# Performance work log

Measured on AMD Instinct MI355X. Metric: run time of the kernel, lower is better.

Reference implementation:

```python
import jax, jax.numpy as jnp
import numpy as np

EPS = 1e-5
TAU = 2.0
HEADS = 8
SCALE = 0.125


def _bn(y, g, b, m, v):
    # y: [TB, C, N]; per-channel eval-mode batchnorm
    inv = jax.lax.rsqrt(v + EPS)
    return (y - m[:, None]) * (g * inv)[:, None] + b[:, None]


def _lif(x_seq, vth):
    # spikingjelly MultiStepLIFNode: v += (x - v)/tau, spike = H(v - vth), hard reset v*(1-s)
    def step(mem, xt):
        mem = mem + (xt - mem) / TAU
        s = (mem >= vth).astype(xt.dtype)
        mem = mem * (1.0 - s)
        return mem, s
    _, spikes = jax.lax.scan(step, jnp.zeros_like(x_seq[0]), x_seq)
    return spikes


def setup_inputs() -> dict:
    key = jax.random.key(0)
    ks = jax.random.split(key, 8)
    T, B, C, H, W = 4, 16, 256, 32, 32
    d = {
        'x': jax.random.normal(ks[0], (T, B, C, H, W), jnp.float32),
        'res_attn': jnp.zeros((1,), jnp.float32),
    }
    for i, p in enumerate(['q', 'k', 'v']):
        d[p + '_w'] = jax.random.normal(ks[1 + i], (C, C), jnp.float32) * 0.02
        d[p + '_gamma'] = jnp.ones((C,), jnp.float32)
        d[p + '_beta'] = jnp.zeros((C,), jnp.float32)
        d[p + '_mean'] = jnp.zeros((C,), jnp.float32)
        d[p + '_var'] = jnp.ones((C,), jnp.float32)
    d['p_w'] = jax.random.normal(ks[4], (C, C), jnp.float32) * 0.02
    d['p_b'] = jnp.zeros((C,), jnp.float32)
    d['p_gamma'] = jnp.ones((C,), jnp.float32)
    d['p_beta'] = jnp.zeros((C,), jnp.float32)
    d['p_mean'] = jnp.zeros((C,), jnp.float32)
    d['p_var'] = jnp.ones((C,), jnp.float32)
    return d


def reference(x, res_attn, q_w, q_gamma, q_beta, q_mean, q_var,
              k_w, k_gamma, k_beta, k_mean, k_var,
              v_w, v_gamma, v_beta, v_mean, v_var,
              p_w, p_b, p_gamma, p_beta, p_mean, p_var):
    T, B, C, H, W = x.shape
    N = H * W
    d = C // HEADS
    x2 = x.reshape(T * B, C, N)

    def branch(w, g, b, m, v):
        y = _bn(jnp.einsum('oc,bcn->bon', w, x2), g, b, m, v).reshape(T, B, C, N)
        s = _lif(y, 1.0)  # [T,B,C,N]
        # -> [T,B,heads,N,d]
        return s.transpose(0, 1, 3, 2).reshape(T, B, N, HEADS, d).transpose(0, 1, 3, 2, 4)

    q = branch(q_w, q_gamma, q_beta, q_mean, q_var)
    k = branch(k_w, k_gamma, k_beta, k_mean, k_var)
    v = branch(v_w, v_gamma, v_beta, v_mean, v_var)

    kv = jnp.einsum('tbhnd,tbhne->tbhde', k, v)      # [T,B,h,d,d]
    attn = jnp.einsum('tbhnd,tbhde->tbhne', q, kv) * SCALE  # [T,B,h,N,d]
    xa = attn.transpose(0, 1, 2, 4, 3).reshape(T, B, C, N)
    xa = _lif(xa, 0.5)

    y = _bn(jnp.einsum('oc,bcn->bon', p_w, xa.reshape(T * B, C, N)) + p_b[:, None],
            p_gamma, p_beta, p_mean, p_var)
    out = _lif(y.reshape(T, B, C, H, W), 1.0)
    return (out, v)
```

## Files before the change

### kernel.cpp

```cpp
#include <hip/hip_runtime.h>
#include <stdint.h>

typedef unsigned int u32;
typedef unsigned short ushort_t;

#define T_ 4
#define B_ 16
#define C_ 256
#define N_ 1024
#define CN (C_ * N_)
#define M_ELEMS (64 * C_ * N_)

#define OFF_S    0ull
#define OFF_YP   0ull
#define OFF_XC   67108864ull
#define OFF_SC   67108864ull
#define OFF_KV   134217728ull
#define OFF_BNS  136314880ull
#define OFF_WC   136331264ull
#define OFF_WPC  137510912ull

typedef __attribute__((ext_vector_type(8))) short bf16x8;
typedef __attribute__((ext_vector_type(4))) float f32x4;

__device__ __forceinline__ ushort_t f2bf(float f) {
  u32 u = __float_as_uint(f);
  u32 r = (u + 0x7FFFu + ((u >> 16) & 1u)) >> 16;
  return (ushort_t)r;
}
__device__ __forceinline__ float bf2f(ushort_t h) { return __uint_as_float((u32)h << 16); }

__device__ __forceinline__ void async_copy16(const void* g, void* l) {
  __builtin_amdgcn_global_load_lds(
      (const __attribute__((address_space(1))) u32*)g,
      (__attribute__((address_space(3))) u32*)l, 16, 0, 0);
}

__device__ __forceinline__ void mfma_grp(const ushort_t* Ap, int aoff,
                                         bf16x8 b0, bf16x8 b1, bf16x8 b2, bf16x8 b3,
                                         f32x4* acc) {
  bf16x8 a0 = *(const bf16x8*)&Ap[aoff + 0 * 16 * 32];
  bf16x8 a1 = *(const bf16x8*)&Ap[aoff + 1 * 16 * 32];
  bf16x8 a2 = *(const bf16x8*)&Ap[aoff + 2 * 16 * 32];
  bf16x8 a3 = *(const bf16x8*)&Ap[aoff + 3 * 16 * 32];
  acc[0]  = __builtin_amdgcn_mfma_f32_16x16x32_bf16(a0, b0, acc[0],  0, 0, 0);
  acc[1]  = __builtin_amdgcn_mfma_f32_16x16x32_bf16(a0, b1, acc[1],  0, 0, 0);
  acc[2]  = __builtin_amdgcn_mfma_f32_16x16x32_bf16(a0, b2, acc[2],  0, 0, 0);
  acc[3]  = __builtin_amdgcn_mfma_f32_16x16x32_bf16(a0, b3, acc[3],  0, 0, 0);
  acc[4]  = __builtin_amdgcn_mfma_f32_16x16x32_bf16(a1, b0, acc[4],  0, 0, 0);
  acc[5]  = __builtin_amdgcn_mfma_f32_16x16x32_bf16(a1, b1, acc[5],  0, 0, 0);
  acc[6]  = __builtin_amdgcn_mfma_f32_16x16x32_bf16(a1, b2, acc[6],  0, 0, 0);
  acc[7]  = __builtin_amdgcn_mfma_f32_16x16x32_bf16(a1, b3, acc[7],  0, 0, 0);
  acc[8]  = __builtin_amdgcn_mfma_f32_16x16x32_bf16(a2, b0, acc[8],  0, 0, 0);
  acc[9]  = __builtin_amdgcn_mfma_f32_16x16x32_bf16(a2, b1, acc[9],  0, 0, 0);
  acc[10] = __builtin_amdgcn_mfma_f32_16x16x32_bf16(a2, b2, acc[10], 0, 0, 0);
  acc[11] = __builtin_amdgcn_mfma_f32_16x16x32_bf16(a2, b3, acc[11], 0, 0, 0);
  acc[12] = __builtin_amdgcn_mfma_f32_16x16x32_bf16(a3, b0, acc[12], 0, 0, 0);
  acc[13] = __builtin_amdgcn_mfma_f32_16x16x32_bf16(a3, b1, acc[13], 0, 0, 0);
  acc[14] = __builtin_amdgcn_mfma_f32_16x16x32_bf16(a3, b2, acc[14], 0, 0, 0);
  acc[15] = __builtin_amdgcn_mfma_f32_16x16x32_bf16(a3, b3, acc[15], 0, 0, 0);
}

__global__ void bn_prep(const float* __restrict__ qg, const float* __restrict__ qb2, const float* __restrict__ qm, const float* __restrict__ qv,
                        const float* __restrict__ kg, const float* __restrict__ kb, const float* __restrict__ km, const float* __restrict__ kvv,
                        const float* __restrict__ vg, const float* __restrict__ vb, const float* __restrict__ vm, const float* __restrict__ vv,
                        const float* __restrict__ pbias,
                        const float* __restrict__ pg, const float* __restrict__ pbt, const float* __restrict__ pm, const float* __restrict__ pv,
                        float* __restrict__ bns) {
  int i = threadIdx.x;
  int br = i >> 8, c = i & 255;
  const float *g, *bt, *m, *v;
  float bias = 0.f;
  if (br == 0)      { g = qg; bt = qb2; m = qm; v = qv; }
  else if (br == 1) { g = kg; bt = kb;  m = km; v = kvv; }
  else if (br == 2) { g = vg; bt = vb;  m = vm; v = vv; }
  else              { g = pg; bt = pbt; m = pm; v = pv; bias = pbias[c]; }
  float sc = g[c] / sqrtf(v[c] + 1e-5f);
  float sh = bt[c] + (bias - m[c]) * sc;
  float rcp = (sc != 0.f) ? (1.f / sc) : 0.f;
  *(float4*)&bns[4 * i] = make_float4(sc, sh, rcp, 0.f);
}

__global__ __launch_bounds__(256) void convert_w(const float* __restrict__ qw, const float* __restrict__ kw,
                                                 const float* __restrict__ vw, const float* __restrict__ pw,
                                                 ushort_t* __restrict__ Wc, ushort_t* __restrict__ Wpc) {
  int id = blockIdx.x * 256 + threadIdx.x;
  int br = id >> 16, o = (id >> 8) & 255, c = id & 255;
  const float* w = (br == 0) ? qw : (br == 1) ? kw : (br == 2) ? vw : pw;
  float f = w[o * 256 + c];
  ushort_t hi = f2bf(f);
  ushort_t lo = f2bf(f - bf2f(hi));
  if (br < 3) {
    ushort_t* d = Wc + (size_t)br * 196608 + (size_t)o * 768 + c;
    d[0] = hi; d[256] = lo; d[512] = hi;
  } else {
    ushort_t* d = Wpc + (size_t)o * 512 + c;
    d[0] = hi; d[256] = lo;
  }
}

__global__ __launch_bounds__(256) void convert_x(const float* __restrict__ x, ushort_t* __restrict__ Xc) {
  __shared__ ushort_t hi[32][260];
  __shared__ ushort_t lo[32][260];
  int bid = blockIdx.x;
  int nc = bid & 3, kb = (bid >> 2) & 7, tb = bid >> 5;
  int t = threadIdx.x;
  int n0 = nc * 256;
  const float* xb = x + (size_t)tb * CN + (size_t)(kb * 32) * N_ + n0;
#pragma unroll
  for (int p = 0; p < 8; ++p) {
    int k = p * 4 + (t >> 6);
    int n4 = (t & 63) * 4;
    float4 v = *(const float4*)&xb[(size_t)k * N_ + n4];
    ushort_t h0 = f2bf(v.x), h1 = f2bf(v.y), h2 = f2bf(v.z), h3 = f2bf(v.w);
    short4 hv = make_short4((short)h0, (short)h1, (short)h2, (short)h3);
    short4 lv = make_short4((short)f2bf(v.x - bf2f(h0)), (short)f2bf(v.y - bf2f(h1)),
                            (short)f2bf(v.z - bf2f(h2)), (short)f2bf(v.w - bf2f(h3)));
    *(short4*)&hi[k][n4] = hv;
    *(short4*)&lo[k][n4] = lv;
  }
  __syncthreads();
  ushort_t* Hs = Xc + ((size_t)(tb * 16 + kb) * 1024 + n0) * 32;
  ushort_t* Ls = Xc + ((size_t)(tb * 16 + 8 + kb) * 1024 + n0) * 32;
  int kq = t & 3;
#pragma unroll
  for (int q = 0; q < 4; ++q) {
    int n = q * 64 + (t >> 2);
    u32 a0 = (u32)hi[kq * 8 + 0][n] | ((u32)hi[kq * 8 + 1][n] << 16);
    u32 a1 = (u32)hi[kq * 8 + 2][n] | ((u32)hi[kq * 8 + 3][n] << 16);
    u32 a2 = (u32)hi[kq * 8 + 4][n] | ((u32)hi[kq * 8 + 5][n] << 16);
    u32 a3 = (u32)hi[kq * 8 + 6][n] | ((u32)hi[kq * 8 + 7][n] << 16);
    *(uint4*)(Hs + (size_t)n * 32 + kq * 8) = make_uint4(a0, a1, a2, a3);
    u32 b0 = (u32)lo[kq * 8 + 0][n] | ((u32)lo[kq * 8 + 1][n] << 16);
    u32 b1 = (u32)lo[kq * 8 + 2][n] | ((u32)lo[kq * 8 + 3][n] << 16);
    u32 b2 = (u32)lo[kq * 8 + 4][n] | ((u32)lo[kq * 8 + 5][n] << 16);
    u32 b3 = (u32)lo[kq * 8 + 6][n] | ((u32)lo[kq * 8 + 7][n] << 16);
    *(uint4*)(Ls + (size_t)n * 32 + kq * 8) = make_uint4(b0, b1, b2, b3);
  }
}

__global__ __launch_bounds__(256, 3) void gemm_qkv_lif(
    const ushort_t* __restrict__ Wc, const ushort_t* __restrict__ Xc,
    const float* __restrict__ bns, uint8_t* __restrict__ S) {
  __shared__ ushort_t Ah[2][4096];
  __shared__ ushort_t Xl[2][4096];
  __shared__ ushort_t Bh[2][4096];
  const int nt = blockIdx.x, mt = blockIdx.y, b = blockIdx.z;
  const int br = mt >> 1, rh = mt & 1;
  const ushort_t* Ab = Wc + (size_t)br * 196608 + (size_t)(rh * 128) * 768;
  const int tid = threadIdx.x;
  const int lane = tid & 63;
  const int quad = lane >> 4, r = lane & 15;
  const int w = tid >> 6;
  const int moff = (w & 1) * 64, noff = (w >> 1) * 64;
  const int c0 = tid, c1 = tid + 256;
  const int aoff = (moff + r) * 32 + quad * 8;
  const int boff = (noff + r) * 32 + quad * 8;

  f32x4 acc[16];
#pragma unroll
  for (int f = 0; f < 16; ++f) acc[f] = (f32x4){0.f, 0.f, 0.f, 0.f};

  for (int t = 0; t < 4; ++t) {
    const ushort_t* Xtb = Xc + (size_t)(t * 16 + b) * 16 * 32768 + (size_t)(nt * 128) * 32;
    for (int p = 0; p < 4; ++p) {
      const ushort_t* AcH = Ab + p * 64;
      const ushort_t* AcL = Ab + 256 + p * 64;
      const ushort_t* Bh0 = Xtb + (size_t)(2 * p) * 32768;
      const ushort_t* Bh1 = Bh0 + 32768;
      async_copy16(AcH + (size_t)(c0 >> 2) * 768 + (c0 & 3) * 8,      &Ah[0][c0 * 8]);
      async_copy16(AcH + (size_t)(c1 >> 2) * 768 + (c1 & 3) * 8,      &Ah[0][c1 * 8]);
      async_copy16(AcH + (size_t)(c0 >> 2) * 768 + 32 + (c0 & 3) * 8, &Ah[1][c0 * 8]);
      async_copy16(AcH + (size_t)(c1 >> 2) * 768 + 32 + (c1 & 3) * 8, &Ah[1][c1 * 8]);
      async_copy16(AcL + (size_t)(c0 >> 2) * 768 + (c0 & 3) * 8,      &Xl[0][c0 * 8]);
      async_copy16(AcL + (size_t)(c1 >> 2) * 768 + (c1 & 3) * 8,      &Xl[0][c1 * 8]);
      async_copy16(AcL + (size_t)(c0 >> 2) * 768 + 32 + (c0 & 3) * 8, &Xl[1][c0 * 8]);
      async_copy16(AcL + (size_t)(c1 >> 2) * 768 + 32 + (c1 & 3) * 8, &Xl[1][c1 * 8]);
      async_copy16(Bh0 + c0 * 8, &Bh[0][c0 * 8]);
      async_copy16(Bh0 + c1 * 8, &Bh[0][c1 * 8]);
      async_copy16(Bh1 + c0 * 8, &Bh[1][c0 * 8]);
      async_copy16(Bh1 + c1 * 8, &Bh[1][c1 * 8]);
      __syncthreads();
      {
        bf16x8 b0 = *(const bf16x8*)&Bh[0][boff + 0 * 16 * 32];
        bf16x8 b1 = *(const bf16x8*)&Bh[0][boff + 1 * 16 * 32];
        bf16x8 b2 = *(const bf16x8*)&Bh[0][boff + 2 * 16 * 32];
        bf16x8 b3 = *(const bf16x8*)&Bh[0][boff + 3 * 16 * 32];
        mfma_grp(&Ah[0][0], aoff, b0, b1, b2, b3, acc);
        mfma_grp(&Xl[0][0], aoff, b0, b1, b2, b3, acc);
      }
      {
        bf16x8 b0 = *(const bf16x8*)&Bh[1][boff + 0 * 16 * 32];
        bf16x8 b1 = *(const bf16x8*)&Bh[1][boff + 1 * 16 * 32];
        bf16x8 b2 = *(const bf16x8*)&Bh[1][boff + 2 * 16 * 32];
        bf16x8 b3 = *(const bf16x8*)&Bh[1][boff + 3 * 16 * 32];
        mfma_grp(&Ah[1][0], aoff, b0, b1, b2, b3, acc);
        mfma_grp(&Xl[1][0], aoff, b0, b1, b2, b3, acc);
      }
      __syncthreads();
      const ushort_t* Bl0 = Xtb + (size_t)(8 + 2 * p) * 32768;
      const ushort_t* Bl1 = Bl0 + 32768;
      async_copy16(Bl0 + c0 * 8, &Xl[0][c0 * 8]);
      async_copy16(Bl0 + c1 * 8, &Xl[0][c1 * 8]);
      async_copy16(Bl1 + c0 * 8, &Xl[1][c0 * 8]);
      async_copy16(Bl1 + c1 * 8, &Xl[1][c1 * 8]);
      __syncthreads();
      {
        bf16x8 b0 = *(const bf16x8*)&Xl[0][boff + 0 * 16 * 32];
        bf16x8 b1 = *(const bf16x8*)&Xl[0][boff + 1 * 16 * 32];
        bf16x8 b2 = *(const bf16x8*)&Xl[0][boff + 2 * 16 * 32];
        bf16x8 b3 = *(const bf16x8*)&Xl[0][boff + 3 * 16 * 32];
        mfma_grp(&Ah[0][0], aoff, b0, b1, b2, b3, acc);
      }
      {
        bf16x8 b0 = *(const bf16x8*)&Xl[1][boff + 0 * 16 * 32];
        bf16x8 b1 = *(const bf16x8*)&Xl[1][boff + 1 * 16 * 32];
        bf16x8 b2 = *(const bf16x8*)&Xl[1][boff + 2 * 16 * 32];
        bf16x8 b3 = *(const bf16x8*)&Xl[1][boff + 3 * 16 * 32];
        mfma_grp(&Ah[1][0], aoff, b0, b1, b2, b3, acc);
      }
      __syncthreads();
    }
    uint8_t* Sb = S + (size_t)br * M_ELEMS + (size_t)(t * 16 + b) * CN;
#pragma unroll
    for (int i = 0; i < 4; ++i) {
#pragma unroll
      for (int rg = 0; rg < 4; ++rg) {
        int c = rh * 128 + moff + i * 16 + quad * 4 + rg;
        float4 bn = *(const float4*)&bns[4 * (br * 256 + c)];
        float hsc = 0.5f * bn.x;
        float hsh = 0.5f * bn.y;
        float rcp = bn.z;
        uint8_t* row = Sb + (size_t)c * N_ + nt * 128 + noff + r;
#pragma unroll
        for (int j = 0; j < 4; ++j) {
          float m = acc[i * 4 + j][rg] * hsc + hsh;
          uint8_t s = (m >= 1.0f) ? 1 : 0;
          row[j * 16] = s;
          acc[i * 4 + j][rg] = s ? 0.f : m * rcp;
        }
      }
    }
  }
}

__global__ __launch_bounds__(256) void transpose_v(const uint8_t* __restrict__ SV, float* __restrict__ vout) {
  size_t o4 = ((size_t)blockIdx.x * 256 + threadIdx.x) * 4;
  int dd = (int)(o4 & 31);
  int n = (int)((o4 >> 5) & 1023);
  int h = (int)((o4 >> 15) & 7);
  int tb = (int)(o4 >> 18);
  const uint8_t* src = SV + (size_t)tb * CN + (size_t)(h * 32 + dd) * N_ + n;
  *(float4*)(vout + o4) = make_float4((float)src[0], (float)src[(size_t)N_],
                                      (float)src[2 * (size_t)N_], (float)src[3 * (size_t)N_]);
}

__global__ __launch_bounds__(256) void kv_gram(const uint8_t* __restrict__ SK,
                                               const uint8_t* __restrict__ SV,
                                               float* __restrict__ KV) {
  __shared__ uint8_t Ks[32 * 132];
  __shared__ uint8_t Vs[32 * 132];
  const int tb = blockIdx.x >> 3, h = blockIdx.x & 7;
  const uint8_t* K = SK + (size_t)tb * CN + (size_t)h * 32 * N_;
  const uint8_t* V = SV + (size_t)tb * CN + (size_t)h * 32 * N_;
  const int tid = threadIdx.x;
  const int dd = tid >> 3, e0 = (tid & 7) * 4;
  const int lr = tid >> 3, lc = (tid & 7) * 16;
  float a0 = 0.f, a1 = 0.f, a2 = 0.f, a3 = 0.f;
  for (int n0 = 0; n0 < N_; n0 += 128) {
    uint4 kk4 = *(const uint4*)(K + (size_t)lr * N_ + n0 + lc);
    uint4 vv4 = *(const uint4*)(V + (size_t)lr * N_ + n0 + lc);
    unsigned* Kw = (unsigned*)(Ks + lr * 132 + lc);
    unsigned* Vw = (unsigned*)(Vs + lr * 132 + lc);
    Kw[0] = kk4.x; Kw[1] = kk4.y; Kw[2] = kk4.z; Kw[3] = kk4.w;
    Vw[0] = vv4.x; Vw[1] = vv4.y; Vw[2] = vv4.z; Vw[3] = vv4.w;
    __syncthreads();
    for (int n = 0; n < 128; ++n) {
      float kf = (float)Ks[dd * 132 + n];
      a0 += kf * (float)Vs[(e0 + 0) * 132 + n];
      a1 += kf * (float)Vs[(e0 + 1) * 132 + n];
      a2 += kf * (float)Vs[(e0 + 2) * 132 + n];
      a3 += kf * (float)Vs[(e0 + 3) * 132 + n];
    }
    __syncthreads();
  }
  float* o = KV + (size_t)(tb * 8 + h) * 1024 + dd * 32 + e0;
  o[0] = a0; o[1] = a1; o[2] = a2; o[3] = a3;
}

__global__ __launch_bounds__(256) void attn_lif(const uint8_t* __restrict__ SQ,
                                                const float* __restrict__ KV,
                                                ushort_t* __restrict__ Sc) {
  __shared__ float kvs[1024];
  const int bid = blockIdx.x;
  const int nb = bid & 15, h = (bid >> 4) & 7, b = bid >> 7;
  const int n0 = nb * 64;
  const int tid = threadIdx.x;
  const int nl = tid & 63, eg = tid >> 6;
  float mem[8];
#pragma unroll
  for (int j = 0; j < 8; ++j) mem[j] = 0.f;
  for (int t = 0; t < 4; ++t) {
    const float* kvp = KV + (size_t)((t * B_ + b) * 8 + h) * 1024;
    *(float4*)&kvs[tid * 4] = *(const float4*)&kvp[tid * 4];
    __syncthreads();
    const uint8_t* q = SQ + (size_t)(t * B_ + b) * CN + (size_t)h * 32 * N_ + n0 + nl;
    float val[8];
#pragma unroll
    for (int j = 0; j < 8; ++j) val[j] = 0.f;
#pragma unroll 4
    for (int dd = 0; dd < 32; ++dd) {
      float qv = (float)q[(size_t)dd * N_];
#pragma unroll
      for (int j = 0; j < 8; ++j) val[j] += qv * kvs[dd * 32 + eg * 8 + j];
    }
    ushort_t pk[8];
#pragma unroll
    for (int j = 0; j < 8; ++j) {
      float a = val[j] * 0.125f;
      mem[j] += (a - mem[j]) * 0.5f;
      int s = (mem[j] >= 0.5f);
      pk[j] = s ? (ushort_t)0x3F80 : (ushort_t)0;
      if (s) mem[j] = 0.f;
    }
    uint4 o;
    o.x = (u32)pk[0] | ((u32)pk[1] << 16);
    o.y = (u32)pk[2] | ((u32)pk[3] << 16);
    o.z = (u32)pk[4] | ((u32)pk[5] << 16);
    o.w = (u32)pk[6] | ((u32)pk[7] << 16);
    *(uint4*)(Sc + ((size_t)((t * B_ + b) * 8 + h) * 1024 + n0 + nl) * 32 + eg * 8) = o;
    __syncthreads();
  }
}

__global__ __launch_bounds__(256, 3) void gemm_p_mfma(
    const ushort_t* __restrict__ Wpc, const ushort_t* __restrict__ Sc,
    const float* __restrict__ bns, float* __restrict__ YP) {
  __shared__ ushort_t Ah[2][4096];
  __shared__ ushort_t Al[2][4096];
  __shared__ ushort_t Bs[2][4096];
  const int nt = blockIdx.x, mt = blockIdx.y, tb = blockIdx.z;
  const ushort_t* Ab = Wpc + (size_t)(mt * 128) * 512;
  const int tid = threadIdx.x;
  const int lane = tid & 63;
  const int quad = lane >> 4, r = lane & 15;
  const int w = tid >> 6;
  const int moff = (w & 1) * 64, noff = (w >> 1) * 64;
  const int c0 = tid, c1 = tid + 256;
  const int aoff = (moff + r) * 32 + quad * 8;
  const int boff = (noff + r) * 32 + quad * 8;
  f32x4 acc[16];
#pragma unroll
  for (int f = 0; f < 16; ++f) acc[f] = (f32x4){0.f, 0.f, 0.f, 0.f};
  const ushort_t* Stb = Sc + (size_t)tb * 8 * 32768 + (size_t)(nt * 128) * 32;
  for (int p = 0; p < 4; ++p) {
    const ushort_t* AcH = Ab + p * 64;
    const ushort_t* AcL = Ab + 256 + p * 64;
    const ushort_t* Bb0 = Stb + (size_t)(2 * p) * 32768;
    const ushort_t* Bb1 = Bb0 + 32768;
    async_copy16(AcH + (size_t)(c0 >> 2) * 512 + (c0 & 3) * 8,      &Ah[0][c0 * 8]);
    async_copy16(AcH + (size_t)(c1 >> 2) * 512 + (c1 & 3) * 8,      &Ah[0][c1 * 8]);
    async_copy16(AcH + (size_t)(c0 >> 2) * 512 + 32 + (c0 & 3) * 8, &Ah[1][c0 * 8]);
    async_copy16(AcH + (size_t)(c1 >> 2) * 512 + 32 + (c1 & 3) * 8, &Ah[1][c1 * 8]);
    async_copy16(AcL + (size_t)(c0 >> 2) * 512 + (c0 & 3) * 8,      &Al[0][c0 * 8]);
    async_copy16(AcL + (size_t)(c1 >> 2) * 512 + (c1 & 3) * 8,      &Al[0][c1 * 8]);
    async_copy16(AcL + (size_t)(c0 >> 2) * 512 + 32 + (c0 & 3) * 8, &Al[1][c0 * 8]);
    async_copy16(AcL + (size_t)(c1 >> 2) * 512 + 32 + (c1 & 3) * 8, &Al[1][c1 * 8]);
    async_copy16(Bb0 + c0 * 8, &Bs[0][c0 * 8]);
    async_copy16(Bb0 + c1 * 8, &Bs[0][c1 * 8]);
    async_copy16(Bb1 + c0 * 8, &Bs[1][c0 * 8]);
    async_copy16(Bb1 + c1 * 8, &Bs[1][c1 * 8]);
    __syncthreads();
    {
      bf16x8 b0 = *(const bf16x8*)&Bs[0][boff + 0 * 16 * 32];
      bf16x8 b1 = *(const bf16x8*)&Bs[0][boff + 1 * 16 * 32];
      bf16x8 b2 = *(const bf16x8*)&Bs[0][boff + 2 * 16 * 32];
      bf16x8 b3 = *(const bf16x8*)&Bs[0][boff + 3 * 16 * 32];
      mfma_grp(&Ah[0][0], aoff, b0, b1, b2, b3, acc);
      mfma_grp(&Al[0][0], aoff, b0, b1, b2, b3, acc);
    }
    {
      bf16x8 b0 = *(const bf16x8*)&Bs[1][boff + 0 * 16 * 32];
      bf16x8 b1 = *(const bf16x8*)&Bs[1][boff + 1 * 16 * 32];
      bf16x8 b2 = *(const bf16x8*)&Bs[1][boff + 2 * 16 * 32];
      bf16x8 b3 = *(const bf16x8*)&Bs[1][boff + 3 * 16 * 32];
      mfma_grp(&Ah[1][0], aoff, b0, b1, b2, b3, acc);
      mfma_grp(&Al[1][0], aoff, b0, b1, b2, b3, acc);
    }
    __syncthreads();
  }
  float* Yb = YP + (size_t)tb * CN;
#pragma unroll
  for (int i = 0; i < 4; ++i) {
#pragma unroll
    for (int rg = 0; rg < 4; ++rg) {
      int c = mt * 128 + moff + i * 16 + quad * 4 + rg;
      float4 bn = *(const float4*)&bns[4 * (768 + c)];
      float sc = bn.x;
      float sh = bn.y;
      float* row = Yb + (size_t)c * N_ + nt * 128 + noff + r;
#pragma unroll
      for (int j = 0; j < 4; ++j) row[j * 16] = acc[i * 4 + j][rg] * sc + sh;
    }
  }
}

__global__ __launch_bounds__(256) void lif_out(const float* __restrict__ YP, float* __restrict__ out) {
  size_t e4 = ((size_t)blockIdx.x * 256 + threadIdx.x) * 4;
  float m0 = 0.f, m1 = 0.f, m2 = 0.f, m3 = 0.f;
#pragma unroll
  for (int t = 0; t < 4; ++t) {
    float4 y = *(const float4*)(YP + (size_t)t * (B_ * CN) + e4);
    m0 += (y.x - m0) * 0.5f;
    m1 += (y.y - m1) * 0.5f;
    m2 += (y.z - m2) * 0.5f;
    m3 += (y.w - m3) * 0.5f;
    float s0 = (m0 >= 1.0f) ? 1.f : 0.f;
    float s1 = (m1 >= 1.0f) ? 1.f : 0.f;
    float s2 = (m2 >= 1.0f) ? 1.f : 0.f;
    float s3 = (m3 >= 1.0f) ? 1.f : 0.f;
    *(float4*)(out + (size_t)t * (B_ * CN) + e4) = make_float4(s0, s1, s2, s3);
    m0 *= (1.f - s0);
    m1 *= (1.f - s1);
    m2 *= (1.f - s2);
    m3 *= (1.f - s3);
  }
}

extern "C" void kernel_launch(void* const* d_in, const int* in_sizes, int n_in,
                              void* d_out, int out_size, void* d_ws, size_t ws_size,
                              hipStream_t stream) {
  const float* x   = (const float*)d_in[0];
  const float* qw  = (const float*)d_in[2];
  const float* qg  = (const float*)d_in[3];
  const float* qb  = (const float*)d_in[4];
  const float* qm  = (const float*)d_in[5];
  const float* qv  = (const float*)d_in[6];
  const float* kw  = (const float*)d_in[7];
  const float* kg  = (const float*)d_in[8];
  const float* kb  = (const float*)d_in[9];
  const float* km  = (const float*)d_in[10];
  const float* kvv = (const float*)d_in[11];
  const float* vw  = (const float*)d_in[12];
  const float* vg  = (const float*)d_in[13];
  const float* vb  = (const float*)d_in[14];
  const float* vm  = (const float*)d_in[15];
  const float* vv  = (const float*)d_in[16];
  const float* pw  = (const float*)d_in[17];
  const float* pb  = (const float*)d_in[18];
  const float* pg  = (const float*)d_in[19];
  const float* pbt = (const float*)d_in[20];
  const float* pm  = (const float*)d_in[21];
  const float* pv  = (const float*)d_in[22];

  float* out = (float*)d_out;
  float* vout = out + M_ELEMS;

  uint8_t* ws = (uint8_t*)d_ws;
  uint8_t* S   = ws + OFF_S;
  float* YP    = (float*)(ws + OFF_YP);
  ushort_t* Xc = (ushort_t*)(ws + OFF_XC);
  ushort_t* Sc = (ushort_t*)(ws + OFF_SC);
  float* KV    = (float*)(ws + OFF_KV);
  float* BNS   = (float*)(ws + OFF_BNS);
  ushort_t* Wc  = (ushort_t*)(ws + OFF_WC);
  ushort_t* Wpc = (ushort_t*)(ws + OFF_WPC);

  bn_prep<<<dim3(1), dim3(1024), 0, stream>>>(qg, qb, qm, qv, kg, kb, km, kvv,
                                              vg, vb, vm, vv, pb, pg, pbt, pm, pv, BNS);
  convert_w<<<dim3(1024), dim3(256), 0, stream>>>(qw, kw, vw, pw, Wc, Wpc);
  convert_x<<<dim3(2048), dim3(256), 0, stream>>>(x, Xc);
  gemm_qkv_lif<<<dim3(8, 6, 16), dim3(256), 0, stream>>>(Wc, Xc, BNS, S);
  transpose_v<<<dim3(16384), dim3(256), 0, stream>>>(S + 2ull * M_ELEMS, vout);
  kv_gram<<<dim3(512), dim3(256), 0, stream>>>(S + 1ull * M_ELEMS, S + 2ull * M_ELEMS, KV);
  attn_lif<<<dim3(2048), dim3(256), 0, stream>>>(S, KV, Sc);
  gemm_p_mfma<<<dim3(8, 2, 64), dim3(256), 0, stream>>>(Wpc, Sc, BNS, YP);
  lif_out<<<dim3(4096), dim3(256), 0, stream>>>(YP, out);
}
```

Measured before the change: 433.9 us.

## Fuse output LIF into projection GEMM and bit-pack spikes for KV gram

The projection GEMM now loops over the four timesteps inside one block per batch and applies BN plus the LIF recurrence in its epilogue, keeping membrane state in the accumulators. This removes the fp32 YP intermediate round trip and the separate lif_out kernel. The kv_gram kernel packs byte spikes into 64-bit bitmasks and computes K^T V with AND plus popcount instead of a float loop over bytes. The trade-off is a GEMM grid four times smaller (256 blocks), which may underfill the GPU. The fused epilogue also relies on the bns table holding a reciprocal scale in its z field to carry the membrane between timesteps.

```diff
diff --git a/kernel.cpp b/kernel.cpp
--- a/kernel.cpp
+++ b/kernel.cpp
@@ -12,7 +12,6 @@
 #define M_ELEMS (64 * C_ * N_)
 
 #define OFF_S    0ull
-#define OFF_YP   0ull
 #define OFF_XC   67108864ull
 #define OFF_SC   67108864ull
 #define OFF_KV   134217728ull
@@ -258,34 +257,36 @@
 __global__ __launch_bounds__(256) void kv_gram(const uint8_t* __restrict__ SK,
                                                const uint8_t* __restrict__ SV,
                                                float* __restrict__ KV) {
-  __shared__ uint8_t Ks[32 * 132];
-  __shared__ uint8_t Vs[32 * 132];
+  __shared__ unsigned long long Kb[32][17];
+  __shared__ unsigned long long Vb[32][17];
   const int tb = blockIdx.x >> 3, h = blockIdx.x & 7;
   const uint8_t* K = SK + (size_t)tb * CN + (size_t)h * 32 * N_;
   const uint8_t* V = SV + (size_t)tb * CN + (size_t)h * 32 * N_;
   const int tid = threadIdx.x;
+  const int row = tid >> 3, c8 = tid & 7;
+  uint8_t* Kb8 = (uint8_t*)&Kb[row][0];
+  uint8_t* Vb8 = (uint8_t*)&Vb[row][0];
+#pragma unroll
+  for (int i = 0; i < 16; ++i) {
+    int c = c8 + 8 * i;
+    unsigned long long xk = *(const unsigned long long*)(K + (size_t)row * N_ + (size_t)c * 8);
+    unsigned long long xv = *(const unsigned long long*)(V + (size_t)row * N_ + (size_t)c * 8);
+    Kb8[c] = (uint8_t)((xk * 0x8040201008040201ull) >> 56);
+    Vb8[c] = (uint8_t)((xv * 0x8040201008040201ull) >> 56);
+  }
+  __syncthreads();
   const int dd = tid >> 3, e0 = (tid & 7) * 4;
-  const int lr = tid >> 3, lc = (tid & 7) * 16;
-  float a0 = 0.f, a1 = 0.f, a2 = 0.f, a3 = 0.f;
-  for (int n0 = 0; n0 < N_; n0 += 128) {
-    uint4 kk4 = *(const uint4*)(K + (size_t)lr * N_ + n0 + lc);
-    uint4 vv4 = *(const uint4*)(V + (size_t)lr * N_ + n0 + lc);
-    unsigned* Kw = (unsigned*)(Ks + lr * 132 + lc);
-    unsigned* Vw = (unsigned*)(Vs + lr * 132 + lc);
-    Kw[0] = kk4.x; Kw[1] = kk4.y; Kw[2] = kk4.z; Kw[3] = kk4.w;
-    Vw[0] = vv4.x; Vw[1] = vv4.y; Vw[2] = vv4.z; Vw[3] = vv4.w;
-    __syncthreads();
-    for (int n = 0; n < 128; ++n) {
-      float kf = (float)Ks[dd * 132 + n];
-      a0 += kf * (float)Vs[(e0 + 0) * 132 + n];
-      a1 += kf * (float)Vs[(e0 + 1) * 132 + n];
-      a2 += kf * (float)Vs[(e0 + 2) * 132 + n];
-      a3 += kf * (float)Vs[(e0 + 3) * 132 + n];
-    }
-    __syncthreads();
+  int a0 = 0, a1 = 0, a2 = 0, a3 = 0;
+#pragma unroll
+  for (int c = 0; c < 16; ++c) {
+    unsigned long long kd = Kb[dd][c];
+    a0 += __popcll(kd & Vb[e0 + 0][c]);
+    a1 += __popcll(kd & Vb[e0 + 1][c]);
+    a2 += __popcll(kd & Vb[e0 + 2][c]);
+    a3 += __popcll(kd & Vb[e0 + 3][c]);
   }
   float* o = KV + (size_t)(tb * 8 + h) * 1024 + dd * 32 + e0;
-  o[0] = a0; o[1] = a1; o[2] = a2; o[3] = a3;
+  o[0] = (float)a0; o[1] = (float)a1; o[2] = (float)a2; o[3] = (float)a3;
 }
 
 __global__ __launch_bounds__(256) void attn_lif(const uint8_t* __restrict__ SQ,
@@ -333,13 +334,13 @@
   }
 }
 
-__global__ __launch_bounds__(256, 3) void gemm_p_mfma(
+__global__ __launch_bounds__(256, 3) void gemm_p_lif(
     const ushort_t* __restrict__ Wpc, const ushort_t* __restrict__ Sc,
-    const float* __restrict__ bns, float* __restrict__ YP) {
+    const float* __restrict__ bns, float* __restrict__ out) {
   __shared__ ushort_t Ah[2][4096];
   __shared__ ushort_t Al[2][4096];
   __shared__ ushort_t Bs[2][4096];
-  const int nt = blockIdx.x, mt = blockIdx.y, tb = blockIdx.z;
+  const int nt = blockIdx.x, mt = blockIdx.y, b = blockIdx.z;
   const ushort_t* Ab = Wpc + (size_t)(mt * 128) * 512;
   const int tid = threadIdx.x;
   const int lane = tid & 63;
@@ -352,78 +353,65 @@
   f32x4 acc[16];
 #pragma unroll
   for (int f = 0; f < 16; ++f) acc[f] = (f32x4){0.f, 0.f, 0.f, 0.f};
-  const ushort_t* Stb = Sc + (size_t)tb * 8 * 32768 + (size_t)(nt * 128) * 32;
-  for (int p = 0; p < 4; ++p) {
-    const ushort_t* AcH = Ab + p * 64;
-    const ushort_t* AcL = Ab + 256 + p * 64;
-    const ushort_t* Bb0 = Stb + (size_t)(2 * p) * 32768;
-    const ushort_t* Bb1 = Bb0 + 32768;
-    async_copy16(AcH + (size_t)(c0 >> 2) * 512 + (c0 & 3) * 8,      &Ah[0][c0 * 8]);
-    async_copy16(AcH + (size_t)(c1 >> 2) * 512 + (c1 & 3) * 8,      &Ah[0][c1 * 8]);
-    async_copy16(AcH + (size_t)(c0 >> 2) * 512 + 32 + (c0 & 3) * 8, &Ah[1][c0 * 8]);
-    async_copy16(AcH + (size_t)(c1 >> 2) * 512 + 32 + (c1 & 3) * 8, &Ah[1][c1 * 8]);
-    async_copy16(AcL + (size_t)(c0 >> 2) * 512 + (c0 & 3) * 8,      &Al[0][c0 * 8]);
-    async_copy16(AcL + (size_t)(c1 >> 2) * 512 + (c1 & 3) * 8,      &Al[0][c1 * 8]);
-    async_copy16(AcL + (size_t)(c0 >> 2) * 512 + 32 + (c0 & 3) * 8, &Al[1][c0 * 8]);
-    async_copy16(AcL + (size_t)(c1 >> 2) * 512 + 32 + (c1 & 3) * 8, &Al[1][c1 * 8]);
-    async_copy16(Bb0 + c0 * 8, &Bs[0][c0 * 8]);
-    async_copy16(Bb0 + c1 * 8, &Bs[0][c1 * 8]);
-    async_copy16(Bb1 + c0 * 8, &Bs[1][c0 * 8]);
-    async_copy16(Bb1 + c1 * 8, &Bs[1][c1 * 8]);
-    __syncthreads();
-    {
-      bf16x8 b0 = *(const bf16x8*)&Bs[0][boff + 0 * 16 * 32];
-      bf16x8 b1 = *(const bf16x8*)&Bs[0][boff + 1 * 16 * 32];
-      bf16x8 b2 = *(const bf16x8*)&Bs[0][boff + 2 * 16 * 32];
-      bf16x8 b3 = *(const bf16x8*)&Bs[0][boff + 3 * 16 * 32];
-      mfma_grp(&Ah[0][0], aoff, b0, b1, b2, b3, acc);
-      mfma_grp(&Al[0][0], aoff, b0, b1, b2, b3, acc);
-    }
-    {
-      bf16x8 b0 = *(const bf16x8*)&Bs[1][boff + 0 * 16 * 32];
-      bf16x8 b1 = *(const bf16x8*)&Bs[1][boff + 1 * 16 * 32];
-      bf16x8 b2 = *(const bf16x8*)&Bs[1][boff + 2 * 16 * 32];
-      bf16x8 b3 = *(const bf16x8*)&Bs[1][boff + 3 * 16 * 32];
-      mfma_grp(&Ah[1][0], aoff, b0, b1, b2, b3, acc);
-      mfma_grp(&Al[1][0], aoff, b0, b1, b2, b3, acc);
-    }
-    __syncthreads();
-  }
-  float* Yb = YP + (size_t)tb * CN;
-#pragma unroll
-  for (int i = 0; i < 4; ++i) {
-#pragma unroll
-    for (int rg = 0; rg < 4; ++rg) {
-      int c = mt * 128 + moff + i * 16 + quad * 4 + rg;
-      float4 bn = *(const float4*)&bns[4 * (768 + c)];
-      float sc = bn.x;
-      float sh = bn.y;
-      float* row = Yb + (size_t)c * N_ + nt * 128 + noff + r;
-#pragma unroll
-      for (int j = 0; j < 4; ++j) row[j * 16] = acc[i * 4 + j][rg] * sc + sh;
-    }
-  }
-}
-
-__global__ __launch_bounds__(256) void lif_out(const float* __restrict__ YP, float* __restrict__ out) {
-  size_t e4 = ((size_t)blockIdx.x * 256 + threadIdx.x) * 4;
-  float m0 = 0.f, m1 = 0.f, m2 = 0.f, m3 = 0.f;
-#pragma unroll
+
   for (int t = 0; t < 4; ++t) {
-    float4 y = *(const float4*)(YP + (size_t)t * (B_ * CN) + e4);
-    m0 += (y.x - m0) * 0.5f;
-    m1 += (y.y - m1) * 0.5f;
-    m2 += (y.z - m2) * 0.5f;
-    m3 += (y.w - m3) * 0.5f;
-    float s0 = (m0 >= 1.0f) ? 1.f : 0.f;
-    float s1 = (m1 >= 1.0f) ? 1.f : 0.f;
-    float s2 = (m2 >= 1.0f) ? 1.f : 0.f;
-    float s3 = (m3 >= 1.0f) ? 1.f : 0.f;
-    *(float4*)(out + (size_t)t * (B_ * CN) + e4) = make_float4(s0, s1, s2, s3);
-    m0 *= (1.f - s0);
-    m1 *= (1.f - s1);
-    m2 *= (1.f - s2);
-    m3 *= (1.f - s3);
+    const ushort_t* Stb = Sc + (size_t)(t * 16 + b) * 8 * 32768 + (size_t)(nt * 128) * 32;
+    for (int p = 0; p < 4; ++p) {
+      const ushort_t* AcH = Ab + p * 64;
+      const ushort_t* AcL = Ab + 256 + p * 64;
+      const ushort_t* Bb0 = Stb + (size_t)(2 * p) * 32768;
+      const ushort_t* Bb1 = Bb0 + 32768;
+      async_copy16(AcH + (size_t)(c0 >> 2) * 512 + (c0 & 3) * 8,      &Ah[0][c0 * 8]);
+      async_copy16(AcH + (size_t)(c1 >> 2) * 512 + (c1 & 3) * 8,      &Ah[0][c1 * 8]);
+      async_copy16(AcH + (size_t)(c0 >> 2) * 512 + 32 + (c0 & 3) * 8, &Ah[1][c0 * 8]);
+      async_copy16(AcH + (size_t)(c1 >> 2) * 512 + 32 + (c1 & 3) * 8, &Ah[1][c1 * 8]);
+      async_copy16(AcL + (size_t)(c0 >> 2) * 512 + (c0 & 3) * 8,      &Al[0][c0 * 8]);
+      async_copy16(AcL + (size_t)(c1 >> 2) * 512 + (c1 & 3) * 8,      &Al[0][c1 * 8]);
+      async_copy16(AcL + (size_t)(c0 >> 2) * 512 + 32 + (c0 & 3) * 8, &Al[1][c0 * 8]);
+      async_copy16(AcL + (size_t)(c1 >> 2) * 512 + 32 + (c1 & 3) * 8, &Al[1][c1 * 8]);
+      async_copy16(Bb0 + c0 * 8, &Bs[0][c0 * 8]);
+      async_copy16(Bb0 + c1 * 8, &Bs[0][c1 * 8]);
+      async_copy16(Bb1 + c0 * 8, &Bs[1][c0 * 8]);
+      async_copy16(Bb1 + c1 * 8, &Bs[1][c1 * 8]);
+      __syncthreads();
+      {
+        bf16x8 b0 = *(const bf16x8*)&Bs[0][boff + 0 * 16 * 32];
+        bf16x8 b1 = *(const bf16x8*)&Bs[0][boff + 1 * 16 * 32];
+        bf16x8 b2 = *(const bf16x8*)&Bs[0][boff + 2 * 16 * 32];
+        bf16x8 b3 = *(const bf16x8*)&Bs[0][boff + 3 * 16 * 32];
+        mfma_grp(&Ah[0][0], aoff, b0, b1, b2, b3, acc);
+        mfma_grp(&Al[0][0], aoff, b0, b1, b2, b3, acc);
+      }
+      {
+        bf16x8 b0 = *(const bf16x8*)&Bs[1][boff + 0 * 16 * 32];
+        bf16x8 b1 = *(const bf16x8*)&Bs[1][boff + 1 * 16 * 32];
+        bf16x8 b2 = *(const bf16x8*)&Bs[1][boff + 2 * 16 * 32];
+        bf16x8 b3 = *(const bf16x8*)&Bs[1][boff + 3 * 16 * 32];
+        mfma_grp(&Ah[1][0], aoff, b0, b1, b2, b3, acc);
+        mfma_grp(&Al[1][0], aoff, b0, b1, b2, b3, acc);
+      }
+      __syncthreads();
+    }
+    float* Ob = out + (size_t)(t * 16 + b) * CN;
+#pragma unroll
+    for (int i = 0; i < 4; ++i) {
+#pragma unroll
+      for (int rg = 0; rg < 4; ++rg) {
+        int c = mt * 128 + moff + i * 16 + quad * 4 + rg;
+        float4 bn = *(const float4*)&bns[4 * (768 + c)];
+        float hsc = 0.5f * bn.x;
+        float hsh = 0.5f * bn.y;
+        float rcp = bn.z;
+        float* row = Ob + (size_t)c * N_ + nt * 128 + noff + r;
+#pragma unroll
+        for (int j = 0; j < 4; ++j) {
+          float m = acc[i * 4 + j][rg] * hsc + hsh;
+          int s = (m >= 1.0f);
+          row[j * 16] = s ? 1.0f : 0.0f;
+          acc[i * 4 + j][rg] = s ? 0.f : m * rcp;
+        }
+      }
+    }
   }
 }
 
@@ -458,7 +446,6 @@
 
   uint8_t* ws = (uint8_t*)d_ws;
   uint8_t* S   = ws + OFF_S;
-  float* YP    = (float*)(ws + OFF_YP);
   ushort_t* Xc = (ushort_t*)(ws + OFF_XC);
   ushort_t* Sc = (ushort_t*)(ws + OFF_SC);
   float* KV    = (float*)(ws + OFF_KV);
@@ -474,6 +461,5 @@
   transpose_v<<<dim3(16384), dim3(256), 0, stream>>>(S + 2ull * M_ELEMS, vout);
   kv_gram<<<dim3(512), dim3(256), 0, stream>>>(S + 1ull * M_ELEMS, S + 2ull * M_ELEMS, KV);
   attn_lif<<<dim3(2048), dim3(256), 0, stream>>>(S, KV, Sc);
-  gemm_p_mfma<<<dim3(8, 2, 64), dim3(256), 0, stream>>>(Wpc, Sc, BNS, YP);
-  lif_out<<<dim3(4096), dim3(256), 0, stream>>>(YP, out);
-}
+  gemm_p_lif<<<dim3(8, 2, 16), dim3(256), 0, stream>>>(Wpc, Sc, BNS, out);
+}
```

After: 403.1 us. -7.1%, faster.
